# Optimization experiments

Hardware: AMD Instinct MI355X
Metric: run time of the kernel (lower is better)

Reference implementation:

```python
import jax, jax.numpy as jnp
import numpy as np

BITS = 4
MASK = (1 << BITS) - 1  # 15


def _dequant(qweight, scales, qzeros, groupsize):
    # qweight: [in//32*bits, out] int32; 8 nibbles packed per int32 along rows.
    out_f = qweight.shape[1]
    shifts = jnp.arange(0, 32, BITS, dtype=jnp.int32)  # [8]
    # [rows, 8, out] -> unpacked int weights in [0, 15]
    w = (qweight[:, None, :] >> shifts[None, :, None]) & MASK
    w = w.reshape(-1, groupsize, out_f)  # [n_groups, groupsize, out]
    s = scales.reshape(-1, 1, out_f)     # [n_groups, 1, out]
    z = qzeros.reshape(-1, 1, out_f)
    W = s * w.astype(scales.dtype) - z * s
    return W.reshape(-1, out_f)          # [in, out]


def setup_inputs() -> dict:
    key = jax.random.key(0)
    k1, k2, k3, k4, k5 = jax.random.split(key, 5)
    B, S, IN, OUT, G = 4, 2048, 4096, 4096, 64
    x = jax.random.normal(k1, (B, S, IN), dtype=jnp.float16)
    qweight = jax.random.randint(k2, (IN // 32 * BITS, OUT), 0, 2147483647, dtype=jnp.int32)
    scales = (jax.random.uniform(k3, (IN // G, OUT), dtype=jnp.float32) * 0.01 + 0.001).astype(jnp.float16)
    qzeros = (jax.random.uniform(k4, (IN // G, OUT), dtype=jnp.float32) * 15.0).astype(jnp.float16)
    bias = jax.random.normal(k5, (OUT,), dtype=jnp.float16)
    return {"x": x, "qweight": qweight, "scales": scales, "qzeros": qzeros,
            "bias": bias, "groupsize": G, "bits": BITS}


def reference(x, qweight, scales, qzeros, bias, groupsize, bits):
    W = _dequant(qweight, scales, qzeros, groupsize)  # [in, out] fp16
    return jnp.matmul(x, W) + bias
```

## Files before the change

kernel.cpp:

```cpp
#include <hip/hip_runtime.h>
#include <stdint.h>
#include <stddef.h>

typedef __bf16 bf16;
typedef __bf16 bf16x8 __attribute__((ext_vector_type(8)));
typedef float  f32x4  __attribute__((ext_vector_type(4)));

#define GLOBAL_AS(p) ((const __attribute__((address_space(1))) void*)(p))
#define LDS_AS(p)    ((__attribute__((address_space(3))) void*)(p))

__device__ __forceinline__ void gload_lds16(const bf16* g, bf16* l) {
    __builtin_amdgcn_global_load_lds(GLOBAL_AS(g), LDS_AS(l), 16, 0, 0);
}

__global__ __launch_bounds__(256)
void convert_x_kernel(const float* __restrict__ x, bf16* __restrict__ xb, long n8) {
    long t = (long)blockIdx.x * blockDim.x + threadIdx.x;
    if (t >= n8) return;
    const f32x4* p = (const f32x4*)(x + t * 8);
    f32x4 a = p[0], b = p[1];
    bf16x8 v;
#pragma unroll
    for (int j = 0; j < 4; ++j) { v[j] = (bf16)a[j]; v[4 + j] = (bf16)b[j]; }
    *(bf16x8*)(xb + t * 8) = v;
}

__global__ __launch_bounds__(256)
void dequant_wt_tiled_kernel(const uint32_t* __restrict__ qw,
                             const float* __restrict__ scales,
                             const float* __restrict__ qzeros,
                             bf16* __restrict__ Wt,
                             int N, int K, int rows_per_group) {
    const int i = blockIdx.x * 256 + threadIdx.x;
    const int w = i >> 6, l = i & 63;
    const int nrq = K >> 5;
    const int rq = w % nrq;
    const int o  = (w / nrq) * 16 + (l >> 2);
    const int c  = l & 3;
    const int r  = rq * 4 + c;
    if (o >= N) return;
    const uint32_t q = qw[(size_t)r * N + o];
    const int g = r / rows_per_group;
    const float s = scales[(size_t)g * N + o];
    const float z = qzeros[(size_t)g * N + o];
    const float nsz = -s * z;
    bf16x8 v;
#pragma unroll
    for (int j = 0; j < 8; ++j)
        v[j] = (bf16)fmaf((float)((q >> (4 * j)) & 15u), s, nsz);
    *(bf16x8*)(Wt + (size_t)rq * N * 32 + (size_t)o * 32 + c * 8) = v;
}

constexpr int BM = 128, BN = 128, BK = 32;

template <bool FUSED>
__global__ __launch_bounds__(256)
void gemm_kernel(const bf16* __restrict__ Ab,
                 const float* __restrict__ Af,
                 const bf16* __restrict__ Bt,
                 const uint32_t* __restrict__ qw,
                 const float* __restrict__ scales,
                 const float* __restrict__ qzeros,
                 const float* __restrict__ bias,
                 float* __restrict__ out,
                 int M, int N, int K, int G) {
    __shared__ __align__(16) bf16 As[BM * BK];
    __shared__ __align__(16) bf16 Bs[BN * BK];

    const int tid  = threadIdx.x;
    const int lane = tid & 63;
    const int wave = tid >> 6;
    const int wm = wave & 1;
    const int wn = wave >> 1;
    const int m0 = blockIdx.y * BM;
    const int n0 = blockIdx.x * BN;

    const int lrow = lane & 15;
    const int lk8  = (lane >> 4) * 8;

    f32x4 acc[4][4];
#pragma unroll
    for (int i = 0; i < 4; ++i)
#pragma unroll
        for (int j = 0; j < 4; ++j) acc[i][j] = (f32x4){0.f, 0.f, 0.f, 0.f};

    for (int kt = 0; kt < K; kt += BK) {
        if (!FUSED) {
            const bf16* bsrc = Bt + (size_t)(kt >> 5) * N * 32 + (size_t)n0 * 32;
#pragma unroll
            for (int it = 0; it < 2; ++it) {
                const int c = tid + it * 256;
                const int row = c >> 2;
                const int kc  = (c & 3) * 8;
                gload_lds16(Ab + (size_t)(m0 + row) * K + kt + kc, As + c * 8);
                gload_lds16(bsrc + c * 8, Bs + c * 8);
            }
        } else {
#pragma unroll
            for (int it = 0; it < 2; ++it) {
                const int c = tid + it * 256;
                const int row = c >> 2;
                const int kc  = (c & 3) * 8;
                const f32x4* p = (const f32x4*)(Af + (size_t)(m0 + row) * K + kt + kc);
                f32x4 a = p[0], b = p[1];
                bf16x8 v;
#pragma unroll
                for (int j = 0; j < 4; ++j) { v[j] = (bf16)a[j]; v[4 + j] = (bf16)b[j]; }
                *(bf16x8*)(As + row * BK + kc) = v;
            }
            const int g = kt / G;
#pragma unroll
            for (int it = 0; it < 2; ++it) {
                const int idx = tid + it * 256;
                const int rl = idx >> 7;
                const int nl = idx & 127;
                uint32_t q = qw[(size_t)(kt / 8 + rl) * N + n0 + nl];
                float s = scales[(size_t)g * N + n0 + nl];
                float z = qzeros[(size_t)g * N + n0 + nl];
                float nsz = -s * z;
                bf16x8 v;
#pragma unroll
                for (int j = 0; j < 8; ++j)
                    v[j] = (bf16)fmaf((float)((q >> (4 * j)) & 15u), s, nsz);
                *(bf16x8*)(Bs + nl * BK + rl * 8) = v;
            }
        }
        __syncthreads();

        bf16x8 a[4], b[4];
#pragma unroll
        for (int i = 0; i < 4; ++i)
            a[i] = *(const bf16x8*)(As + (wm * 64 + i * 16 + lrow) * BK + lk8);
#pragma unroll
        for (int j = 0; j < 4; ++j)
            b[j] = *(const bf16x8*)(Bs + (wn * 64 + j * 16 + lrow) * BK + lk8);

#pragma unroll
        for (int i = 0; i < 4; ++i)
#pragma unroll
            for (int j = 0; j < 4; ++j)
                acc[i][j] = __builtin_amdgcn_mfma_f32_16x16x32_bf16(
                    a[i], b[j], acc[i][j], 0, 0, 0);
        __syncthreads();
    }

#pragma unroll
    for (int j = 0; j < 4; ++j) {
        const int col = n0 + wn * 64 + j * 16 + (lane & 15);
        const float bv = bias[col];
#pragma unroll
        for (int i = 0; i < 4; ++i) {
            const int rbase = m0 + wm * 64 + i * 16 + (lane >> 4) * 4;
#pragma unroll
            for (int r = 0; r < 4; ++r)
                out[(size_t)(rbase + r) * N + col] = acc[i][j][r] + bv;
        }
    }
}

extern "C" void kernel_launch(void* const* d_in, const int* in_sizes, int n_in,
                              void* d_out, int out_size, void* d_ws, size_t ws_size,
                              hipStream_t stream) {
    const float*    x      = (const float*)d_in[0];
    const uint32_t* qw     = (const uint32_t*)d_in[1];
    const float*    scales = (const float*)d_in[2];
    const float*    qzeros = (const float*)d_in[3];
    const float*    bias   = (const float*)d_in[4];
    float*          out    = (float*)d_out;

    const int N = in_sizes[4];
    const int K = (in_sizes[1] / N) * 8;
    const int M = in_sizes[0] / K;
    const int G = K / (in_sizes[2] / N);

    dim3 grid(N / BN, M / BM);
    const size_t xb_bytes = (size_t)M * K * sizeof(bf16);
    const size_t wt_bytes = (size_t)N * K * sizeof(bf16);

    if (ws_size >= xb_bytes + wt_bytes) {
        bf16* Xb = (bf16*)d_ws;
        bf16* Wt = (bf16*)((char*)d_ws + xb_bytes);
        const long n8 = (long)M * K / 8;
        convert_x_kernel<<<(int)((n8 + 255) / 256), 256, 0, stream>>>(x, Xb, n8);
        const long dq_threads = ((long)N / 16) * (K >> 5) * 64;
        dequant_wt_tiled_kernel<<<(int)((dq_threads + 255) / 256), 256, 0, stream>>>(
            qw, scales, qzeros, Wt, N, K, G / 8);
        gemm_kernel<false><<<grid, 256, 0, stream>>>(
            Xb, nullptr, Wt, nullptr, scales, qzeros, bias, out, M, N, K, G);
    } else {
        gemm_kernel<true><<<grid, 256, 0, stream>>>(
            nullptr, x, nullptr, qw, scales, qzeros, bias, out, M, N, K, G);
    }
}
```

Measured before the change: 553.1 us.

## Replace GEMM with 256x256 double-buffered 8-wave ping-pong kernel and XCD remap

The GEMM is rebuilt around 256x256x64 tiles with 512 threads and double-buffered LDS. Global-to-LDS loads are interleaved with MFMA phases, paced by barriers, setprio and waitcnt. LDS uses an XOR swizzle, and blocks are remapped across the XCDs. The dequant output layout changes to 64-wide K chunks to match the new tile. The goal is to hide memory latency and raise MFMA utilization and data reuse, at the cost of much more complex scheduling, heavy register pressure, and a new shape guard.

```diff
diff --git a/kernel.cpp b/kernel.cpp
--- a/kernel.cpp
+++ b/kernel.cpp
@@ -26,18 +26,18 @@
 }
 
 __global__ __launch_bounds__(256)
-void dequant_wt_tiled_kernel(const uint32_t* __restrict__ qw,
-                             const float* __restrict__ scales,
-                             const float* __restrict__ qzeros,
-                             bf16* __restrict__ Wt,
-                             int N, int K, int rows_per_group) {
+void dequant_wt64_kernel(const uint32_t* __restrict__ qw,
+                         const float* __restrict__ scales,
+                         const float* __restrict__ qzeros,
+                         bf16* __restrict__ Wt,
+                         int N, int K, int rows_per_group) {
     const int i = blockIdx.x * 256 + threadIdx.x;
     const int w = i >> 6, l = i & 63;
-    const int nrq = K >> 5;
-    const int rq = w % nrq;
-    const int o  = (w / nrq) * 16 + (l >> 2);
-    const int c  = l & 3;
-    const int r  = rq * 4 + c;
+    const int nr8 = K >> 6;
+    const int r8 = w % nr8;
+    const int o  = (w / nr8) * 8 + (l >> 3);
+    const int rr = l & 7;
+    const int r  = r8 * 8 + rr;
     if (o >= N) return;
     const uint32_t q = qw[(size_t)r * N + o];
     const int g = r / rows_per_group;
@@ -48,35 +48,218 @@
 #pragma unroll
     for (int j = 0; j < 8; ++j)
         v[j] = (bf16)fmaf((float)((q >> (4 * j)) & 15u), s, nsz);
-    *(bf16x8*)(Wt + (size_t)rq * N * 32 + (size_t)o * 32 + c * 8) = v;
-}
-
-constexpr int BM = 128, BN = 128, BK = 32;
-
-template <bool FUSED>
-__global__ __launch_bounds__(256)
-void gemm_kernel(const bf16* __restrict__ Ab,
-                 const float* __restrict__ Af,
-                 const bf16* __restrict__ Bt,
-                 const uint32_t* __restrict__ qw,
-                 const float* __restrict__ scales,
-                 const float* __restrict__ qzeros,
-                 const float* __restrict__ bias,
-                 float* __restrict__ out,
-                 int M, int N, int K, int G) {
-    __shared__ __align__(16) bf16 As[BM * BK];
-    __shared__ __align__(16) bf16 Bs[BN * BK];
+    *(bf16x8*)(Wt + ((size_t)r8 * N + o) * 64 + rr * 8) = v;
+}
+
+constexpr int BM2 = 256, BN2 = 256, BK2 = 64;
+
+#define PHASE_MID()                                      \
+    __builtin_amdgcn_s_barrier();                        \
+    asm volatile("s_waitcnt lgkmcnt(0)" ::: "memory");   \
+    __builtin_amdgcn_sched_barrier(0);                   \
+    __builtin_amdgcn_s_setprio(1)
+
+#define PHASE_END()                                      \
+    __builtin_amdgcn_s_setprio(0);                       \
+    __builtin_amdgcn_sched_barrier(0);                   \
+    __builtin_amdgcn_s_barrier();                        \
+    __builtin_amdgcn_sched_barrier(0)
+
+#define PHASE_END_VM4()                                  \
+    __builtin_amdgcn_s_setprio(0);                       \
+    __builtin_amdgcn_sched_barrier(0);                   \
+    asm volatile("s_waitcnt vmcnt(4)" ::: "memory");     \
+    __builtin_amdgcn_s_barrier();                        \
+    __builtin_amdgcn_sched_barrier(0)
+
+#define MFMA_HALF(A, B, IBASE)                                             \
+    _Pragma("unroll")                                                      \
+    for (int i_ = 0; i_ < 4; ++i_) {                                       \
+        _Pragma("unroll")                                                  \
+        for (int j_ = 0; j_ < 4; ++j_)                                     \
+            acc[(IBASE) + i_][j_] = __builtin_amdgcn_mfma_f32_16x16x32_bf16( \
+                (A)[(IBASE) + i_], (B)[j_], acc[(IBASE) + i_][j_], 0, 0, 0); \
+    }
+
+__global__ __launch_bounds__(512, 2)
+void gemm8_kernel(const bf16* __restrict__ Ab,
+                  const bf16* __restrict__ Bt,
+                  const float* __restrict__ bias,
+                  float* __restrict__ out,
+                  int M, int N, int K, int nbx) {
+    __shared__ __align__(16) bf16 As[2][BM2 * BK2];
+    __shared__ __align__(16) bf16 Bs[2][BN2 * BK2];
 
     const int tid  = threadIdx.x;
     const int lane = tid & 63;
     const int wave = tid >> 6;
-    const int wm = wave & 1;
-    const int wn = wave >> 1;
+    const int wm = wave >> 2;
+    const int wn = wave & 3;
+
+    const int nwg = gridDim.x;
+    int wg = blockIdx.x;
+    {
+        const int q = nwg >> 3, r = nwg & 7;
+        const int xcd = wg & 7, off = wg >> 3;
+        wg = (xcd < r ? xcd * (q + 1) : r * (q + 1) + (xcd - r) * q) + off;
+    }
+    const int nby = nwg / nbx;
+    const int bx = wg / nby;
+    const int by = wg % nby;
+    const int m0 = by * BM2;
+    const int n0 = bx * BN2;
+
+    const int lrow = lane & 15;
+    const int lhi  = lane >> 4;
+    const int swz  = (lrow >> 1) & 7;
+
+    const int NT = K >> 6;
+    const int NI = NT >> 1;
+
+    auto stageA = [&](int tIdx, int half, int buf) {
+#pragma unroll
+        for (int it = 0; it < 2; ++it) {
+            const int q  = tid + it * 512;
+            const int rl = q >> 3;
+            const int cl = (q & 7) ^ ((rl >> 1) & 7);
+            gload_lds16(Ab + (size_t)(m0 + half * 128 + rl) * K + tIdx * 64 + cl * 8,
+                        &As[buf][half * 8192 + q * 8]);
+        }
+    };
+    auto stageB = [&](int tIdx, int half, int buf) {
+#pragma unroll
+        for (int it = 0; it < 2; ++it) {
+            const int q  = tid + it * 512;
+            const int rl = q >> 3;
+            const int cl = (q & 7) ^ ((rl >> 1) & 7);
+            gload_lds16(Bt + ((size_t)tIdx * N + n0 + half * 128 + rl) * 64 + cl * 8,
+                        &Bs[buf][half * 8192 + q * 8]);
+        }
+    };
+
+    f32x4 acc[8][4];
+#pragma unroll
+    for (int i = 0; i < 8; ++i)
+#pragma unroll
+        for (int j = 0; j < 4; ++j) acc[i][j] = (f32x4){0.f, 0.f, 0.f, 0.f};
+
+    stageA(0, 0, 0); stageA(0, 1, 0); stageB(0, 0, 0); stageB(0, 1, 0);
+    stageA(1, 0, 1); stageA(1, 1, 1);
+    asm volatile("s_waitcnt vmcnt(4)" ::: "memory");
+    __builtin_amdgcn_s_barrier();
+    __builtin_amdgcn_sched_barrier(0);
+
+    bf16x8 a0[8], a1[8], b0[4], b1[4];
+
+    for (int i2 = 0; i2 < NI; ++i2) {
+        const int t0  = 2 * i2;
+        const int tS2 = (t0 + 2 < NT) ? t0 + 2 : NT - 1;
+        const int tS3 = (t0 + 3 < NT) ? t0 + 3 : NT - 1;
+
+#pragma unroll
+        for (int i = 0; i < 8; ++i)
+            a0[i] = *(const bf16x8*)(&As[0][(wm * 128 + i * 16 + lrow) * 64 + ((lhi ^ swz) * 8)]);
+#pragma unroll
+        for (int j = 0; j < 4; ++j)
+            b0[j] = *(const bf16x8*)(&Bs[0][(wn * 64 + j * 16 + lrow) * 64 + ((lhi ^ swz) * 8)]);
+        stageB(t0 + 1, 0, 1);
+        PHASE_MID();
+        MFMA_HALF(a0, b0, 0);
+        PHASE_END();
+
+#pragma unroll
+        for (int i = 0; i < 8; ++i)
+            a1[i] = *(const bf16x8*)(&As[0][(wm * 128 + i * 16 + lrow) * 64 + (((lhi + 4) ^ swz) * 8)]);
+        stageB(t0 + 1, 1, 1);
+        PHASE_MID();
+        MFMA_HALF(a0, b0, 4);
+        PHASE_END();
+
+#pragma unroll
+        for (int j = 0; j < 4; ++j)
+            b1[j] = *(const bf16x8*)(&Bs[0][(wn * 64 + j * 16 + lrow) * 64 + (((lhi + 4) ^ swz) * 8)]);
+        stageA(tS2, 0, 0);
+        PHASE_MID();
+        MFMA_HALF(a1, b1, 0);
+        PHASE_END();
+
+        stageA(tS2, 1, 0);
+        PHASE_MID();
+        MFMA_HALF(a1, b1, 4);
+        PHASE_END_VM4();
+
+#pragma unroll
+        for (int i = 0; i < 8; ++i)
+            a0[i] = *(const bf16x8*)(&As[1][(wm * 128 + i * 16 + lrow) * 64 + ((lhi ^ swz) * 8)]);
+#pragma unroll
+        for (int j = 0; j < 4; ++j)
+            b0[j] = *(const bf16x8*)(&Bs[1][(wn * 64 + j * 16 + lrow) * 64 + ((lhi ^ swz) * 8)]);
+        stageB(tS2, 0, 0);
+        PHASE_MID();
+        MFMA_HALF(a0, b0, 0);
+        PHASE_END();
+
+#pragma unroll
+        for (int i = 0; i < 8; ++i)
+            a1[i] = *(const bf16x8*)(&As[1][(wm * 128 + i * 16 + lrow) * 64 + (((lhi + 4) ^ swz) * 8)]);
+        stageB(tS2, 1, 0);
+        PHASE_MID();
+        MFMA_HALF(a0, b0, 4);
+        PHASE_END();
+
+#pragma unroll
+        for (int j = 0; j < 4; ++j)
+            b1[j] = *(const bf16x8*)(&Bs[1][(wn * 64 + j * 16 + lrow) * 64 + (((lhi + 4) ^ swz) * 8)]);
+        stageA(tS3, 0, 1);
+        PHASE_MID();
+        MFMA_HALF(a1, b1, 0);
+        PHASE_END();
+
+        stageA(tS3, 1, 1);
+        PHASE_MID();
+        MFMA_HALF(a1, b1, 4);
+        PHASE_END_VM4();
+    }
+
+    asm volatile("s_waitcnt vmcnt(0)" ::: "memory");
+
+#pragma unroll
+    for (int j = 0; j < 4; ++j) {
+        const int col = n0 + wn * 64 + j * 16 + lrow;
+        const float bv = bias[col];
+#pragma unroll
+        for (int i = 0; i < 8; ++i) {
+            const int rbase = m0 + wm * 128 + i * 16 + lhi * 4;
+#pragma unroll
+            for (int r = 0; r < 4; ++r)
+                out[(size_t)(rbase + r) * N + col] = acc[i][j][r] + bv;
+        }
+    }
+}
+
+constexpr int BM = 128, BN = 128, BK = 32;
+
+__global__ __launch_bounds__(256)
+void gemm_fused_kernel(const float* __restrict__ Af,
+                       const uint32_t* __restrict__ qw,
+                       const float* __restrict__ scales,
+                       const float* __restrict__ qzeros,
+                       const float* __restrict__ bias,
+                       float* __restrict__ out,
+                       int M, int N, int K, int G) {
+    __shared__ __align__(16) bf16 As2[BM * BK];
+    __shared__ __align__(16) bf16 Bs2[BN * BK];
+
+    const int tid  = threadIdx.x;
+    const int lane = tid & 63;
+    const int wave = tid >> 6;
+    const int wmm = wave & 1;
+    const int wnn = wave >> 1;
     const int m0 = blockIdx.y * BM;
     const int n0 = blockIdx.x * BN;
 
-    const int lrow = lane & 15;
-    const int lk8  = (lane >> 4) * 8;
+    const int lr = lane & 15;
+    const int lk8 = (lane >> 4) * 8;
 
     f32x4 acc[4][4];
 #pragma unroll
@@ -85,55 +268,43 @@
         for (int j = 0; j < 4; ++j) acc[i][j] = (f32x4){0.f, 0.f, 0.f, 0.f};
 
     for (int kt = 0; kt < K; kt += BK) {
-        if (!FUSED) {
-            const bf16* bsrc = Bt + (size_t)(kt >> 5) * N * 32 + (size_t)n0 * 32;
-#pragma unroll
-            for (int it = 0; it < 2; ++it) {
-                const int c = tid + it * 256;
-                const int row = c >> 2;
-                const int kc  = (c & 3) * 8;
-                gload_lds16(Ab + (size_t)(m0 + row) * K + kt + kc, As + c * 8);
-                gload_lds16(bsrc + c * 8, Bs + c * 8);
-            }
-        } else {
-#pragma unroll
-            for (int it = 0; it < 2; ++it) {
-                const int c = tid + it * 256;
-                const int row = c >> 2;
-                const int kc  = (c & 3) * 8;
-                const f32x4* p = (const f32x4*)(Af + (size_t)(m0 + row) * K + kt + kc);
-                f32x4 a = p[0], b = p[1];
-                bf16x8 v;
-#pragma unroll
-                for (int j = 0; j < 4; ++j) { v[j] = (bf16)a[j]; v[4 + j] = (bf16)b[j]; }
-                *(bf16x8*)(As + row * BK + kc) = v;
-            }
-            const int g = kt / G;
-#pragma unroll
-            for (int it = 0; it < 2; ++it) {
-                const int idx = tid + it * 256;
-                const int rl = idx >> 7;
-                const int nl = idx & 127;
-                uint32_t q = qw[(size_t)(kt / 8 + rl) * N + n0 + nl];
-                float s = scales[(size_t)g * N + n0 + nl];
-                float z = qzeros[(size_t)g * N + n0 + nl];
-                float nsz = -s * z;
-                bf16x8 v;
-#pragma unroll
-                for (int j = 0; j < 8; ++j)
-                    v[j] = (bf16)fmaf((float)((q >> (4 * j)) & 15u), s, nsz);
-                *(bf16x8*)(Bs + nl * BK + rl * 8) = v;
-            }
+#pragma unroll
+        for (int it = 0; it < 2; ++it) {
+            const int c = tid + it * 256;
+            const int row = c >> 2;
+            const int kc  = (c & 3) * 8;
+            const f32x4* p = (const f32x4*)(Af + (size_t)(m0 + row) * K + kt + kc);
+            f32x4 a = p[0], b = p[1];
+            bf16x8 v;
+#pragma unroll
+            for (int j = 0; j < 4; ++j) { v[j] = (bf16)a[j]; v[4 + j] = (bf16)b[j]; }
+            *(bf16x8*)(As2 + row * BK + kc) = v;
+        }
+        const int g = kt / G;
+#pragma unroll
+        for (int it = 0; it < 2; ++it) {
+            const int idx = tid + it * 256;
+            const int rl = idx >> 7;
+            const int nl = idx & 127;
+            uint32_t q = qw[(size_t)(kt / 8 + rl) * N + n0 + nl];
+            float s = scales[(size_t)g * N + n0 + nl];
+            float z = qzeros[(size_t)g * N + n0 + nl];
+            float nsz = -s * z;
+            bf16x8 v;
+#pragma unroll
+            for (int j = 0; j < 8; ++j)
+                v[j] = (bf16)fmaf((float)((q >> (4 * j)) & 15u), s, nsz);
+            *(bf16x8*)(Bs2 + nl * BK + rl * 8) = v;
         }
         __syncthreads();
 
         bf16x8 a[4], b[4];
 #pragma unroll
         for (int i = 0; i < 4; ++i)
-            a[i] = *(const bf16x8*)(As + (wm * 64 + i * 16 + lrow) * BK + lk8);
-#pragma unroll
-        for (int j = 0; j < 4; ++j)
-            b[j] = *(const bf16x8*)(Bs + (wn * 64 + j * 16 + lrow) * BK + lk8);
+            a[i] = *(const bf16x8*)(As2 + (wmm * 64 + i * 16 + lr) * BK + lk8);
+#pragma unroll
+        for (int j = 0; j < 4; ++j)
+            b[j] = *(const bf16x8*)(Bs2 + (wnn * 64 + j * 16 + lr) * BK + lk8);
 
 #pragma unroll
         for (int i = 0; i < 4; ++i)
@@ -146,11 +317,11 @@
 
 #pragma unroll
     for (int j = 0; j < 4; ++j) {
-        const int col = n0 + wn * 64 + j * 16 + (lane & 15);
+        const int col = n0 + wnn * 64 + j * 16 + (lane & 15);
         const float bv = bias[col];
 #pragma unroll
         for (int i = 0; i < 4; ++i) {
-            const int rbase = m0 + wm * 64 + i * 16 + (lane >> 4) * 4;
+            const int rbase = m0 + wmm * 64 + i * 16 + (lane >> 4) * 4;
 #pragma unroll
             for (int r = 0; r < 4; ++r)
                 out[(size_t)(rbase + r) * N + col] = acc[i][j][r] + bv;
@@ -173,22 +344,26 @@
     const int M = in_sizes[0] / K;
     const int G = K / (in_sizes[2] / N);
 
-    dim3 grid(N / BN, M / BM);
     const size_t xb_bytes = (size_t)M * K * sizeof(bf16);
     const size_t wt_bytes = (size_t)N * K * sizeof(bf16);
 
-    if (ws_size >= xb_bytes + wt_bytes) {
+    const bool shape_ok = (M % BM2 == 0) && (N % BN2 == 0) && (K % 128 == 0) &&
+                          (G % 8 == 0);
+
+    if (shape_ok && ws_size >= xb_bytes + wt_bytes) {
         bf16* Xb = (bf16*)d_ws;
         bf16* Wt = (bf16*)((char*)d_ws + xb_bytes);
         const long n8 = (long)M * K / 8;
         convert_x_kernel<<<(int)((n8 + 255) / 256), 256, 0, stream>>>(x, Xb, n8);
-        const long dq_threads = ((long)N / 16) * (K >> 5) * 64;
-        dequant_wt_tiled_kernel<<<(int)((dq_threads + 255) / 256), 256, 0, stream>>>(
+        const long dq_threads = ((long)K >> 6) * (N / 8) * 64;
+        dequant_wt64_kernel<<<(int)((dq_threads + 255) / 256), 256, 0, stream>>>(
             qw, scales, qzeros, Wt, N, K, G / 8);
-        gemm_kernel<false><<<grid, 256, 0, stream>>>(
-            Xb, nullptr, Wt, nullptr, scales, qzeros, bias, out, M, N, K, G);
+        const int nbx = N / BN2;
+        const int nwg = nbx * (M / BM2);
+        gemm8_kernel<<<nwg, 512, 0, stream>>>(Xb, Wt, bias, out, M, N, K, nbx);
     } else {
-        gemm_kernel<true><<<grid, 256, 0, stream>>>(
-            nullptr, x, nullptr, qw, scales, qzeros, bias, out, M, N, K, G);
-    }
-}
+        dim3 grid(N / BN, M / BM);
+        gemm_fused_kernel<<<grid, 256, 0, stream>>>(
+            x, qw, scales, qzeros, bias, out, M, N, K, G);
+    }
+}
```

Measured after the change: 529.1 us. 1.05x faster.
